# Kernel optimization log

Hardware: AMD Instinct MI355X
Metric: run time of the kernel (lower is better)

Reference implementation:

```python
import jax, jax.numpy as jnp
import numpy as np
import math

H, D, HID, L, OUT = 4, 64, 256, 2, 128
N = (2048, 4096, 3072)            # participant, gene, metabolite
IN_DIMS = (512, 768, 384)
# edge types: (src_type, dst_type, relation_index)
ETYPES = ((0, 1, 0), (1, 0, 1), (0, 2, 2), (2, 0, 3))
E_COUNTS = (250000, 250000, 200000, 200000)
SCALE = 1.0 / math.sqrt(D)


def _ln(x, g, b, eps=1e-5):
    m = x.mean(-1, keepdims=True)
    v = ((x - m) ** 2).mean(-1, keepdims=True)
    return (x - m) * jax.lax.rsqrt(v + eps) * g + b


def _cross_attn(qx, kvx, qw, qb, kw, kb, vw, vb, ow, ob):
    # qx: [Nq, HID] feature-node embeds (query); kvx: [Nk, HID] participant embeds
    Nq, Nk = qx.shape[0], kvx.shape[0]
    q = (qx @ qw + qb).reshape(Nq, H, D)
    k = (kvx @ kw + kb).reshape(Nk, H, D)
    v = (kvx @ vw + vb).reshape(Nk, H, D)
    att = jnp.einsum('qhd,khd->hqk', q, k) * SCALE
    p = jax.nn.softmax(att, axis=-1)
    o = jnp.einsum('hqk,khd->qhd', p, v).reshape(Nq, H * D)
    return o @ ow + ob


def _hgt_conv(hs, edges, kw, kb, qw, qb, vw, vb, aw, ab, skip, a_rel, m_rel, p_rel):
    # PyG-style HGTConv: per-type K/Q/V projections, per-relation a_rel/m_rel
    # transforms, segment softmax over all incoming edges per dst node.
    K = [(hs[t] @ kw[t] + kb[t]).reshape(N[t], H, D) for t in range(3)]
    Q = [(hs[t] @ qw[t] + qb[t]).reshape(N[t], H, D) for t in range(3)]
    V = [(hs[t] @ vw[t] + vb[t]).reshape(N[t], H, D) for t in range(3)]
    out = []
    for t in range(3):
        al, ms, ds = [], [], []
        for (s, d, r) in ETYPES:
            if d != t:
                continue
            src_idx, dst_idx = edges[r]
            k_e = jnp.einsum('ehd,hdf->ehf', K[s][src_idx], a_rel[r])  # [E,H,D]
            v_e = jnp.einsum('ehd,hdf->ehf', V[s][src_idx], m_rel[r])  # [E,H,D]
            a = (Q[t][dst_idx] * k_e).sum(-1) * (p_rel[r] * SCALE)     # [E,H]
            al.append(a); ms.append(v_e); ds.append(dst_idx)
        a = jnp.concatenate(al, 0)
        msg = jnp.concatenate(ms, 0)
        dst = jnp.concatenate(ds, 0)
        # numerically stable segment softmax grouped by destination node
        amax = jax.ops.segment_max(a, dst, num_segments=N[t])
        ex = jnp.exp(a - amax[dst])
        den = jax.ops.segment_sum(ex, dst, num_segments=N[t])
        w = ex / den[dst]                                             # [E,H]
        agg = jax.ops.segment_sum(w[..., None] * msg, dst,
                                  num_segments=N[t]).reshape(N[t], H * D)
        o = jax.nn.gelu(agg, approximate=False) @ aw[t] + ab[t]
        g = jax.nn.sigmoid(skip[t])
        out.append(g * o + (1.0 - g) * hs[t])
    return out


def _forward(x_p, x_g, x_m, edges, Win_p, bin_p, Win_g, bin_g, Win_m, bin_m,
             kw, kb, qw, qb, vw, vb, aw, ab, skip, a_rel, m_rel, p_rel,
             ca_qw, ca_qb, ca_kw, ca_kb, ca_vw, ca_vb, ca_ow, ca_ob,
             ln_g, ln_b, outw, outb):
    h = [x_p @ Win_p + bin_p, x_g @ Win_g + bin_g, x_m @ Win_m + bin_m]
    for l in range(L):
        hg = _hgt_conv(h, edges, kw[l], kb[l], qw[l], qb[l], vw[l], vb[l],
                       aw[l], ab[l], skip[l], a_rel[l], m_rel[l], p_rel[l])
        new = []
        for t in range(3):
            nh = hg[t]
            if t != 0:  # non-participant types cross-attend to participants
                c = t - 1
                nh = nh + _cross_attn(h[t], h[0], ca_qw[c], ca_qb[c],
                                      ca_kw[c], ca_kb[c], ca_vw[c], ca_vb[c],
                                      ca_ow[c], ca_ob[c])
            x = _ln(h[t] + nh, ln_g[t], ln_b[t])
            new.append(jax.nn.gelu(x, approximate=False))
        h = new
    return jnp.concatenate([h[t] @ outw[t] + outb[t] for t in range(3)], axis=0)


def setup_inputs() -> dict:
    key = jax.random.key(0)
    ks = iter(jax.random.split(key, 64))
    def nrm(shape, s=0.02):
        return jax.random.normal(next(ks), shape, dtype=jnp.float32) * s
    inp = {}
    inp['x_p'] = jax.random.normal(next(ks), (N[0], IN_DIMS[0]), dtype=jnp.float32)
    inp['x_g'] = jax.random.normal(next(ks), (N[1], IN_DIMS[1]), dtype=jnp.float32)
    inp['x_m'] = jax.random.normal(next(ks), (N[2], IN_DIMS[2]), dtype=jnp.float32)
    names = ('pg', 'gp', 'pm', 'mp')
    for (s, d, r), E in zip(ETYPES, E_COUNTS):
        inp['src_' + names[r]] = jax.random.randint(next(ks), (E,), 0, N[s], dtype=jnp.int32)
        inp['dst_' + names[r]] = jax.random.randint(next(ks), (E,), 0, N[d], dtype=jnp.int32)
    for nm, dim in (('p', 512), ('g', 768), ('m', 384)):
        inp['Win_' + nm] = nrm((dim, HID))
        inp['bin_' + nm] = jnp.zeros((HID,), jnp.float32)
    for nm in ('kw', 'qw', 'vw', 'aw'):
        inp[nm] = nrm((L, 3, HID, HID))
    for nm in ('kb', 'qb', 'vb', 'ab'):
        inp[nm] = jnp.zeros((L, 3, HID), jnp.float32)
    inp['skip'] = jnp.ones((L, 3), jnp.float32)
    inp['a_rel'] = nrm((L, 4, H, D, D), 0.1)
    inp['m_rel'] = nrm((L, 4, H, D, D), 0.1)
    inp['p_rel'] = jnp.ones((L, 4, H), jnp.float32)
    for nm in ('ca_qw', 'ca_kw', 'ca_vw', 'ca_ow'):
        inp[nm] = nrm((2, HID, HID))
    for nm in ('ca_qb', 'ca_kb', 'ca_vb', 'ca_ob'):
        inp[nm] = jnp.zeros((2, HID), jnp.float32)
    inp['ln_g'] = jnp.ones((3, HID), jnp.float32)
    inp['ln_b'] = jnp.zeros((3, HID), jnp.float32)
    inp['outw'] = nrm((3, HID, OUT))
    inp['outb'] = jnp.zeros((3, OUT), jnp.float32)
    return inp


def reference(x_p, x_g, x_m, src_pg, dst_pg, src_gp, dst_gp, src_pm, dst_pm,
              src_mp, dst_mp, Win_p, bin_p, Win_g, bin_g, Win_m, bin_m,
              kw, kb, qw, qb, vw, vb, aw, ab, skip, a_rel, m_rel, p_rel,
              ca_qw, ca_qb, ca_kw, ca_kb, ca_vw, ca_vb, ca_ow, ca_ob,
              ln_g, ln_b, outw, outb):
    edges = ((src_pg, dst_pg), (src_gp, dst_gp), (src_pm, dst_pm), (src_mp, dst_mp))
    return _forward(x_p, x_g, x_m, edges, Win_p, bin_p, Win_g, bin_g, Win_m, bin_m,
                    kw, kb, qw, qb, vw, vb, aw, ab, skip, a_rel, m_rel, p_rel,
                    ca_qw, ca_qb, ca_kw, ca_kb, ca_vw, ca_vb, ca_ow, ca_ob,
                    ln_g, ln_b, outw, outb)
```

## Files before the change

kernel.cpp:

```cpp
#include <hip/hip_runtime.h>
#include <math.h>
#include <stdint.h>
#include <stddef.h>

typedef unsigned short ushort_t;
typedef short  bf16x8 __attribute__((ext_vector_type(8)));
typedef float  f32x4  __attribute__((ext_vector_type(4)));
typedef unsigned short us4 __attribute__((ext_vector_type(4)));
typedef __bf16 bf16p2 __attribute__((ext_vector_type(2)));

static constexpr int NHEAD = 4;
static constexpr int HDIM  = 64;
static constexpr int HIDF  = 256;
static constexpr int OUTF  = 128;
static constexpr int N0 = 2048, N1 = 4096, N2 = 3072;
static constexpr int E_PG = 250000, E_GP = 250000, E_PM = 200000, E_MP = 200000;
static constexpr float ATT_SCALE = 0.125f;
static constexpr float LOG2E = 1.4426950408889634f;
static constexpr int EDGE_ITEMS = 2 * N0 + N1 + N2;
static constexpr int E_TOT = E_GP + E_MP + E_PG + E_PM;

enum { M_STORE = 0, M_ADD = 1, M_SKIP = 2, M_B16 = 3, M_GELU_B16 = 4,
       M_SPLITQ = 5, M_VT = 6, M_STOREBOTH = 7 };

__device__ __forceinline__ float gelu_exact(float x) {
    return 0.5f * x * (1.0f + erff(x * 0.7071067811865476f));
}
__device__ __forceinline__ ushort_t f2bf(float f) {
    unsigned x = __float_as_uint(f);
    return (ushort_t)((x + 0x7fffu + ((x >> 16) & 1u)) >> 16);
}
__device__ __forceinline__ float bflo(unsigned u) { return __uint_as_float(u << 16); }
__device__ __forceinline__ float bfhi(unsigned u) { return __uint_as_float(u & 0xffff0000u); }
__device__ __forceinline__ bf16p2 asbf2(unsigned u) { return __builtin_bit_cast(bf16p2, u); }

struct MGemmDesc { const ushort_t* A; const ushort_t* BT; void* C;
                   const float* bias; const float* skipv; void* H;
                   int M; int K; int mode; float scale; };
template <int NZ> struct MGemmDescArr { MGemmDesc d[NZ]; };

template <int NZ>
__global__ __launch_bounds__(256) void gemm_mfma(MGemmDescArr<NZ> P, int N)
{
    const MGemmDesc g = P.d[blockIdx.z];
    const int bm = blockIdx.y << 7;
    if (bm >= g.M) return;
    const int bn = blockIdx.x << 6;
    const int tid = threadIdx.x, wave = tid >> 6, lane = tid & 63;
    const int l15 = lane & 15, lg = lane >> 4;
    const int K = g.K;
    const ushort_t* arow = g.A + (size_t)(bm + (wave << 5) + l15) * K + (lg << 3);
    const ushort_t* brow = g.BT + (size_t)(bn + l15) * K + (lg << 3);

    f32x4 acc[2][4] = {};
    bf16x8 a0 = *(const bf16x8*)(arow);
    bf16x8 a1 = *(const bf16x8*)(arow + (size_t)16 * K);
    bf16x8 bv[4];
#pragma unroll
    for (int ct = 0; ct < 4; ct++)
        bv[ct] = *(const bf16x8*)(brow + (size_t)(ct << 4) * K);

    for (int k0 = 0; k0 < K; k0 += 32) {
        const bf16x8 ca0 = a0, ca1 = a1;
        bf16x8 cb[4];
#pragma unroll
        for (int ct = 0; ct < 4; ct++) cb[ct] = bv[ct];
        if (k0 + 32 < K) {
            a0 = *(const bf16x8*)(arow + k0 + 32);
            a1 = *(const bf16x8*)(arow + (size_t)16 * K + k0 + 32);
#pragma unroll
            for (int ct = 0; ct < 4; ct++)
                bv[ct] = *(const bf16x8*)(brow + (size_t)(ct << 4) * K + k0 + 32);
        }
#pragma unroll
        for (int ct = 0; ct < 4; ct++) {
            acc[0][ct] = __builtin_amdgcn_mfma_f32_16x16x32_bf16(ca0, cb[ct], acc[0][ct], 0, 0, 0);
            acc[1][ct] = __builtin_amdgcn_mfma_f32_16x16x32_bf16(ca1, cb[ct], acc[1][ct], 0, 0, 0);
        }
    }

    const int mode = g.mode;
    float gblend = 0.f, hblend = 0.f;
    if (mode == M_SKIP) {
        const float sv = g.skipv[0];
        gblend = 1.f / (1.f + expf(-sv));
        hblend = 1.f - gblend;
    }
#pragma unroll
    for (int g2 = 0; g2 < 2; g2++) {
        const int rbase = bm + (wave << 5) + (g2 << 4);
#pragma unroll
        for (int ct = 0; ct < 4; ct++) {
            const int col = bn + (ct << 4) + l15;
            const float bia = g.bias ? g.bias[col] : 0.f;
            if (mode == M_VT) {
                const int rowb = rbase + (lg << 2);
                us4 o;
#pragma unroll
                for (int r = 0; r < 4; r++) o[r] = f2bf(acc[g2][ct][r] + bia);
                *(us4*)((ushort_t*)g.C + (size_t)col * g.M + rowb) = o;
                continue;
            }
#pragma unroll
            for (int r = 0; r < 4; r++) {
                const int row = rbase + (lg << 2) + r;
                const float v = acc[g2][ct][r] + bia;
                if (mode == M_STORE) {
                    ((float*)g.C)[(size_t)row * N + col] = v;
                } else if (mode == M_ADD) {
                    ((float*)g.C)[(size_t)row * N + col] += v;
                } else if (mode == M_SKIP) {
                    ((float*)g.C)[(size_t)row * N + col] =
                        gblend * v + hblend * ((const float*)g.H)[(size_t)row * N + col];
                } else if (mode == M_B16) {
                    ((ushort_t*)g.C)[(size_t)row * N + col] = f2bf(v);
                } else if (mode == M_GELU_B16) {
                    ((ushort_t*)g.C)[(size_t)row * N + col] = f2bf(gelu_exact(v));
                } else if (mode == M_SPLITQ) {
                    ((ushort_t*)g.C)[((size_t)(col >> 6) * g.M + row) * 64 + (col & 63)]
                        = f2bf(v * g.scale);
                } else {
                    ((float*)g.C)[(size_t)row * N + col] = v;
                    ((ushort_t*)g.H)[(size_t)row * N + col] = f2bf(v);
                }
            }
        }
    }
}

struct TWDesc { const float* W; ushort_t* WT; int K; int N; };
template <int ND> struct TWDescArr { TWDesc d[ND]; };
struct QFDesc { const float* ar; const float* qwm; const float* qbv;
                ushort_t* wT; float* bT; };
template <int ND> struct QFDescArr { QFDesc d[ND]; };
struct MXDesc { const float* A; const float* B; ushort_t* out; int Kc; };
template <int ND> struct MXDescArr { MXDesc d[ND]; };

struct PreprocArgs {
    TWDescArr<32> T;
    QFDescArr<8> Q;
    MXDescArr<6> X;
    const float* xa; const float* xg; const float* xm; ushort_t* xb;
    int* cur_all;
};
static constexpr int PB_TW = 1536;
static constexpr int PB_QF = PB_TW + 32;
static constexpr int PB_MX = PB_QF + 3072;
static constexpr int PB_C3 = PB_MX + 5248;
static constexpr int PB_Z  = PB_C3 + 44;

__global__ __launch_bounds__(256) void preproc_kernel(PreprocArgs P)
{
    __shared__ __align__(16) char lsbuf[16640];
    const int b = blockIdx.x, tid = threadIdx.x;
    if (b < PB_TW) {
        const int z = b / 48, rem = b - z * 48;
        const int kx = rem % 12, ny = rem / 12;
        const TWDesc g = P.T.d[z];
        const int k0 = kx << 6, n0 = ny << 6;
        if (k0 >= g.K || n0 >= g.N) return;
        float (*Ls)[65] = (float (*)[65])lsbuf;
        const int c = tid & 63, rq = tid >> 6;
        for (int rr = rq; rr < 64; rr += 4)
            Ls[rr][c] = g.W[(size_t)(k0 + rr) * g.N + n0 + c];
        __syncthreads();
        for (int nn = rq; nn < 64; nn += 4)
            g.WT[(size_t)(n0 + nn) * g.K + k0 + c] = f2bf(Ls[c][nn]);
        return;
    }
    if (b < PB_QF) {
        const int idx = b - PB_TW;
        const int h = idx & 3, z = idx >> 2;
        const QFDesc g = P.Q.d[z];
        float (*arS)[64] = (float (*)[64])lsbuf;
        float* qbS = (float*)(lsbuf + 64 * 64 * 4);
        for (int i = tid; i < 4096; i += 256) arS[i >> 6][i & 63] = g.ar[(h << 12) + i];
        if (tid < 64) qbS[tid] = g.qbv[(h << 6) + tid];
        __syncthreads();
        float qv[64];
        const float* qrow = g.qwm + (size_t)tid * HIDF + (h << 6);
#pragma unroll
        for (int f = 0; f < 64; f++) qv[f] = qrow[f];
#pragma unroll 4
        for (int d = 0; d < 64; d++) {
            float a = 0.f;
#pragma unroll
            for (int f = 0; f < 64; f++) a = fmaf(arS[d][f], qv[f], a);
            g.wT[(size_t)((h << 6) + d) * HIDF + tid] = f2bf(a);
        }
        if (tid < 64) {
            float bb = 0.f;
#pragma unroll
            for (int f = 0; f < 64; f++) bb = fmaf(arS[tid][f], qbS[f], bb);
            g.bT[(h << 6) + tid] = bb;
        }
        return;
    }
    if (b < PB_MX) {
        const int idx0 = b - PB_QF;
        const int x = idx0 & 511, y = idx0 >> 9;
        const MXDesc g = P.X.d[y];
        const int idx = x * 256 + tid;
        if (idx >= 256 * g.Kc) return;
        const int col = idx / g.Kc, k = idx - col * g.Kc;
        const int h = col >> 6, f = col & 63;
        const float* M = g.A;
        int kd = k;
        if (k >= 256) { M = g.B; kd = k - 256; }
        const int hp = kd >> 6, d = kd & 63;
        const float v = (hp == h) ? M[(h << 12) + (d << 6) + f] : 0.f;
        g.out[idx] = f2bf(v);
        return;
    }
    if (b < PB_C3) {
        constexpr int n4a = N0 * 512 / 4, n4b = N1 * 768 / 4, n4c = N2 * 384 / 4;
        int i = (b - PB_MX) * 256 + tid;
        const float* src; int j;
        if (i < n4a) { src = P.xa; j = i; }
        else if (i < n4a + n4b) { src = P.xg; j = i - n4a; }
        else if (i < n4a + n4b + n4c) { src = P.xm; j = i - n4a - n4b; }
        else return;
        float4 v = ((const float4*)src)[j];
        us4 o;
        o[0] = f2bf(v.x); o[1] = f2bf(v.y); o[2] = f2bf(v.z); o[3] = f2bf(v.w);
        *(us4*)(P.xb + (size_t)i * 4) = o;
        return;
    }
    {
        int i = (b - PB_C3) * 256 + tid;
        if (i < 2 * N0 + N1 + N2) P.cur_all[i] = 0;
    }
}

__global__ void count4_kernel(const int* __restrict__ d0, const int* __restrict__ d1,
                              const int* __restrict__ d2, const int* __restrict__ d3,
                              int* __restrict__ c0, int* __restrict__ c1,
                              int* __restrict__ c2, int* __restrict__ c3)
{
    int i = blockIdx.x * 256 + threadIdx.x;
    if (i < E_GP) { atomicAdd(&c0[d0[i]], 1); return; }
    i -= E_GP;
    if (i < E_MP) { atomicAdd(&c1[d1[i]], 1); return; }
    i -= E_MP;
    if (i < E_PG) { atomicAdd(&c2[d2[i]], 1); return; }
    i -= E_PG;
    if (i < E_PM) atomicAdd(&c3[d3[i]], 1);
}

struct ScanDesc { int* cntcur; int N; int* off; };

__global__ __launch_bounds__(256) void scan4_kernel(ScanDesc s0, ScanDesc s1,
                                                    ScanDesc s2, ScanDesc s3)
{
    const ScanDesc g = (blockIdx.x == 0) ? s0 : (blockIdx.x == 1) ? s1
                     : (blockIdx.x == 2) ? s2 : s3;
    int* cntcur = g.cntcur; const int N = g.N; int* off = g.off;
    __shared__ int sums[256];
    const int tid = threadIdx.x;
    const int base = tid * 16;
    int vals[16];
    int s = 0;
#pragma unroll
    for (int j = 0; j < 16; j++) {
        int idx = base + j;
        int c = (idx < N) ? cntcur[idx] : 0;
        vals[j] = s; s += c;
    }
    sums[tid] = s;
    __syncthreads();
    for (int d = 1; d < 256; d <<= 1) {
        int v = (tid >= d) ? sums[tid - d] : 0;
        __syncthreads();
        sums[tid] += v;
        __syncthreads();
    }
    int prefix = (tid > 0) ? sums[tid - 1] : 0;
#pragma unroll
    for (int j = 0; j < 16; j++) {
        int idx = base + j;
        if (idx < N) { int v = prefix + vals[j]; off[idx] = v; cntcur[idx] = v; }
    }
    if (tid == 255) off[N] = sums[255];
}

__global__ void scatter4_kernel(
    const int* __restrict__ s0, const int* __restrict__ d0, int* __restrict__ u0, int* __restrict__ e0,
    const int* __restrict__ s1, const int* __restrict__ d1, int* __restrict__ u1, int* __restrict__ e1,
    const int* __restrict__ s2, const int* __restrict__ d2, int* __restrict__ u2, int* __restrict__ e2,
    const int* __restrict__ s3, const int* __restrict__ d3, int* __restrict__ u3, int* __restrict__ e3)
{
    int i = blockIdx.x * 256 + threadIdx.x;
    if (i < E_GP) { e0[atomicAdd(&u0[d0[i]], 1)] = s0[i]; return; }
    i -= E_GP;
    if (i < E_MP) { e1[atomicAdd(&u1[d1[i]], 1)] = s1[i]; return; }
    i -= E_MP;
    if (i < E_PG) { e2[atomicAdd(&u2[d2[i]], 1)] = s2[i]; return; }
    i -= E_PG;
    if (i < E_PM) e3[atomicAdd(&u3[d3[i]], 1)] = s3[i];
}

__device__ __forceinline__ void edge_seg_v9(
    const bf16p2* __restrict__ qd,
    float* __restrict__ sS,
    float2* __restrict__ wssh,
    const int* __restrict__ es, int i0, int i1,
    const ushort_t* __restrict__ Kt, const ushort_t* __restrict__ Vt,
    float pscale, int lane, int koff,
    float& m, float& plsum, float2& acc)
{
    if (i0 >= i1) return;
    const int seg = lane & 3, eidx = lane >> 2;
    const int epar = lane >> 5;
    const int dpair = (lane & 31) << 1;
    const int kbase_off = koff + (seg << 3);

    bool valid = (i0 + lane) < i1;
    int sidx = valid ? es[i0 + lane] : 0;
    uint4 kv[8];
#pragma unroll
    for (int p = 0; p < 4; p++) {
        const int sp = __shfl(sidx, (p << 4) + eidx);
        const ushort_t* kr = Kt + ((size_t)sp << 8) + kbase_off;
        kv[2 * p]     = *(const uint4*)(kr);
        kv[2 * p + 1] = *(const uint4*)(kr + 32);
    }

    for (int c = i0; c < i1; c += 64) {
        const int e2 = c + 64 + lane;
        const bool valid2 = e2 < i1;
        const int sidx2 = valid2 ? es[e2] : 0;

#pragma unroll
        for (int p = 0; p < 4; p++) {
            const uint4 k0 = kv[2 * p], k1 = kv[2 * p + 1];
            float dp = 0.f;
            dp = __builtin_amdgcn_fdot2_f32_bf16(asbf2(k0.x), qd[0], dp, false);
            dp = __builtin_amdgcn_fdot2_f32_bf16(asbf2(k0.y), qd[1], dp, false);
            dp = __builtin_amdgcn_fdot2_f32_bf16(asbf2(k0.z), qd[2], dp, false);
            dp = __builtin_amdgcn_fdot2_f32_bf16(asbf2(k0.w), qd[3], dp, false);
            dp = __builtin_amdgcn_fdot2_f32_bf16(asbf2(k1.x), qd[4], dp, false);
            dp = __builtin_amdgcn_fdot2_f32_bf16(asbf2(k1.y), qd[5], dp, false);
            dp = __builtin_amdgcn_fdot2_f32_bf16(asbf2(k1.z), qd[6], dp, false);
            dp = __builtin_amdgcn_fdot2_f32_bf16(asbf2(k1.w), qd[7], dp, false);
            dp += __shfl_xor(dp, 1);
            dp += __shfl_xor(dp, 2);
            if (seg == 0) sS[(p << 4) + eidx] = dp;
        }
#pragma unroll
        for (int p = 0; p < 4; p++) {
            const int sp = __shfl(sidx2, (p << 4) + eidx);
            const ushort_t* kr = Kt + ((size_t)sp << 8) + kbase_off;
            kv[2 * p]     = *(const uint4*)(kr);
            kv[2 * p + 1] = *(const uint4*)(kr + 32);
        }

        const float a = valid ? sS[lane] * pscale : -INFINITY;

        float cm = a;
#pragma unroll
        for (int o = 32; o; o >>= 1) cm = fmaxf(cm, __shfl_xor(cm, o));
        const float mn = fmaxf(m, cm);
        const float sc = (m == -INFINITY) ? 0.f : expf(m - mn);
        const float w = valid ? expf(a - mn) : 0.f;
        plsum = plsum * sc + w;
        m = mn;
        wssh[lane] = make_float2(w, __int_as_float(sidx));

        acc.x *= sc; acc.y *= sc;
        float2 aE = make_float2(0.f, 0.f), aO = make_float2(0.f, 0.f);
#pragma unroll
        for (int b = 0; b < 64; b += 16) {
            float2 we[8];
            unsigned vv[8];
#pragma unroll
            for (int j = 0; j < 8; j++) we[j] = wssh[b + (j << 1) + epar];
#pragma unroll
            for (int j = 0; j < 8; j++) {
                const int sj = __float_as_int(we[j].y);
                vv[j] = *(const unsigned*)(Vt + (((size_t)sj) << 8) + koff + dpair);
            }
#pragma unroll
            for (int j = 0; j < 8; j++) {
                const float wj = we[j].x;
                if (j & 1) { aO.x = fmaf(wj, bflo(vv[j]), aO.x);
                             aO.y = fmaf(wj, bfhi(vv[j]), aO.y); }
                else       { aE.x = fmaf(wj, bflo(vv[j]), aE.x);
                             aE.y = fmaf(wj, bfhi(vv[j]), aE.y); }
            }
        }
        acc.x += aE.x + aO.x;
        acc.y += aE.y + aO.y;

        valid = valid2; sidx = sidx2;
    }
}

__global__ __launch_bounds__(256) void edge_attn_v9(
    const float* __restrict__ QpDA, const float* __restrict__ QpDB,
    const float* __restrict__ QpS1, const float* __restrict__ QpS2,
    const int* __restrict__ offGP, const int* __restrict__ esGP,
    const int* __restrict__ offMP, const int* __restrict__ esMP,
    const int* __restrict__ offPG, const int* __restrict__ esPG,
    const int* __restrict__ offPM, const int* __restrict__ esPM,
    const ushort_t* __restrict__ K0t, const ushort_t* __restrict__ V0t,
    const ushort_t* __restrict__ K1t, const ushort_t* __restrict__ V1t,
    const ushort_t* __restrict__ K2t, const ushort_t* __restrict__ V2t,
    const float* __restrict__ prel,
    float* __restrict__ accD, float* __restrict__ mlD,
    ushort_t* __restrict__ out1, ushort_t* __restrict__ out2)
{
    __shared__ float sS[NHEAD][64];
    __shared__ float2 wssh[NHEAD][64];
    const int b = blockIdx.x, tid = threadIdx.x, lane = tid & 63, h = tid >> 6;
    const int koff = h << 6, seg = lane & 3;

    const float* Qp; const int* off; const int* es;
    const ushort_t* Kt; const ushort_t* Vt;
    int node, r, dual = -1;
    if (b < N0)            { node = b;            Qp = QpDA; off = offGP; es = esGP; Kt = K1t; Vt = V1t; r = 1; dual = 0; }
    else if (b < 2 * N0)   { node = b - N0;       Qp = QpDB; off = offMP; es = esMP; Kt = K2t; Vt = V2t; r = 3; dual = 1; }
    else if (b < 2 * N0 + N1) { node = b - 2 * N0;      Qp = QpS1; off = offPG; es = esPG; Kt = K0t; Vt = V0t; r = 0; }
    else                      { node = b - 2 * N0 - N1; Qp = QpS2; off = offPM; es = esPM; Kt = K0t; Vt = V0t; r = 2; }

    const float* qrow = Qp + (size_t)node * HIDF + koff;
    float4 qv[4];
    qv[0] = *(const float4*)(qrow + (seg << 3));
    qv[1] = *(const float4*)(qrow + (seg << 3) + 4);
    qv[2] = *(const float4*)(qrow + 32 + (seg << 3));
    qv[3] = *(const float4*)(qrow + 32 + (seg << 3) + 4);
    bf16p2 qd[8];
#pragma unroll
    for (int i = 0; i < 4; i++) {
        const unsigned p0 = (unsigned)f2bf(qv[i].x) | ((unsigned)f2bf(qv[i].y) << 16);
        const unsigned p1 = (unsigned)f2bf(qv[i].z) | ((unsigned)f2bf(qv[i].w) << 16);
        qd[2 * i]     = asbf2(p0);
        qd[2 * i + 1] = asbf2(p1);
    }
    const float ps = prel[(r << 2) + h] * ATT_SCALE;
    float m = -INFINITY, plsum = 0.f;
    float2 acc = make_float2(0.f, 0.f);
    edge_seg_v9(qd, sS[h], wssh[h], es, off[node], off[node + 1],
                Kt, Vt, ps, lane, koff, m, plsum, acc);
    acc.x += __shfl_xor(acc.x, 32);
    acc.y += __shfl_xor(acc.y, 32);
    float l = plsum;
#pragma unroll
    for (int o = 32; o; o >>= 1) l += __shfl_xor(l, o);

    if (dual >= 0) {
        if (lane < 32)
            *(float2*)(accD + ((size_t)(dual * N0 + node)) * HIDF + koff + ((lane & 31) << 1))
                = acc;
        if (lane == 0) {
            mlD[((size_t)(dual * N0 + node)) * 8 + h * 2 + 0] = m;
            mlD[((size_t)(dual * N0 + node)) * 8 + h * 2 + 1] = l;
        }
    } else {
        const float inv = (l > 0.f) ? 1.f / l : 0.f;
        ushort_t* out = (r == 0) ? out1 : out2;
        if (lane < 32) {
            const unsigned pk = (unsigned)f2bf(acc.x * inv) | ((unsigned)f2bf(acc.y * inv) << 16);
            *(unsigned*)(out + (size_t)node * HIDF + koff + ((lane & 31) << 1)) = pk;
        }
    }
}

__global__ __launch_bounds__(256) void combine0_kernel(
    const float* __restrict__ accD, const float* __restrict__ mlD,
    ushort_t* __restrict__ out0)
{
    const int node = blockIdx.x, col = threadIdx.x;
    const int h = col >> 6;
    const float m0 = mlD[((size_t)node) * 8 + h * 2 + 0];
    const float l0 = mlD[((size_t)node) * 8 + h * 2 + 1];
    const float m1 = mlD[((size_t)(N0 + node)) * 8 + h * 2 + 0];
    const float l1 = mlD[((size_t)(N0 + node)) * 8 + h * 2 + 1];
    const float M = fmaxf(m0, m1);
    const float s0 = (m0 == -INFINITY) ? 0.f : expf(m0 - M);
    const float s1 = (m1 == -INFINITY) ? 0.f : expf(m1 - M);
    const float L = l0 * s0 + l1 * s1;
    const float f0 = (L > 0.f) ? s0 / L : 0.f;
    const float f1 = (L > 0.f) ? s1 / L : 0.f;
    const float a0 = accD[((size_t)node) * HIDF + col];
    const float a1 = accD[((size_t)(N0 + node)) * HIDF + col];
    out0[(size_t)node * 512 + col]       = f2bf(a0 * f0);
    out0[(size_t)node * 512 + 256 + col] = f2bf(a1 * f1);
}

struct FlashDesc { const ushort_t* qh; const ushort_t* kh; const ushort_t* vT;
                   ushort_t* O; int Nq; };
template <int NF> struct FlashDescArr { FlashDesc d[NF]; };

template <int NF>
__global__ __launch_bounds__(256) void flash_ca(FlashDescArr<NF> P, int Nk)
{
    const FlashDesc g = P.d[blockIdx.z];
    const int q0 = blockIdx.x << 5;
    if (q0 >= g.Nq) return;
    __shared__ float mS[4][32], lS[4][32];
    __shared__ __align__(16) char uS[18432];
    ushort_t (*Pl)[32][72] = (ushort_t (*)[32][72])uS;
    float    (*oS)[16][64] = (float (*)[16][64])uS;
    const int head = blockIdx.y;
    const int tid = threadIdx.x, wave = tid >> 6, lane = tid & 63;
    const int l15 = lane & 15, lg = lane >> 4;
    const int Nq = g.Nq;

    bf16x8 qa[2][2];
    {
        const ushort_t* qb0 = g.qh + ((size_t)head * Nq + q0 + l15) * 64 + (lg << 3);
        qa[0][0] = *(const bf16x8*)qb0;
        qa[0][1] = *(const bf16x8*)(qb0 + 32);
        qa[1][0] = *(const bf16x8*)(qb0 + 16 * 64);
        qa[1][1] = *(const bf16x8*)(qb0 + 16 * 64 + 32);
    }
    const ushort_t* kbase = g.kh + (size_t)head * Nk * 64;
    const ushort_t* vbase = g.vT + (size_t)head * 64 * Nk;
    const int kchunk = Nk >> 2;
    const int kbeg = wave * kchunk, kend = kbeg + kchunk;

    f32x4 o[2][4] = {};
    float m[2][4]     = {{-INFINITY,-INFINITY,-INFINITY,-INFINITY},
                         {-INFINITY,-INFINITY,-INFINITY,-INFINITY}};
    float plsum[2][4] = {};

    bf16x8 ka[8];
    {
        const ushort_t* krow = kbase + ((size_t)(kbeg + l15)) * 64 + (lg << 3);
#pragma unroll
        for (int ct = 0; ct < 4; ct++) {
            ka[ct]     = *(const bf16x8*)(krow + (ct << 10));
            ka[4 + ct] = *(const bf16x8*)(krow + (ct << 10) + 32);
        }
    }

    for (int k0 = kbeg; k0 < kend; k0 += 64) {
        bf16x8 vv[8];
        const ushort_t* vrow = vbase + (size_t)l15 * Nk + k0 + (lg << 3);
#pragma unroll
        for (int vt = 0; vt < 4; vt++) {
            vv[vt]     = *(const bf16x8*)(vrow + (size_t)(vt << 4) * Nk);
            vv[4 + vt] = *(const bf16x8*)(vrow + (size_t)(vt << 4) * Nk + 32);
        }
        f32x4 s[2][4] = {};
#pragma unroll
        for (int g2 = 0; g2 < 2; g2++)
#pragma unroll
            for (int ct = 0; ct < 4; ct++)
                s[g2][ct] = __builtin_amdgcn_mfma_f32_16x16x32_bf16(qa[g2][0], ka[ct], s[g2][ct], 0, 0, 0);
#pragma unroll
        for (int g2 = 0; g2 < 2; g2++)
#pragma unroll
            for (int ct = 0; ct < 4; ct++)
                s[g2][ct] = __builtin_amdgcn_mfma_f32_16x16x32_bf16(qa[g2][1], ka[4 + ct], s[g2][ct], 0, 0, 0);
        if (k0 + 64 < kend) {
            const ushort_t* krow2 = kbase + ((size_t)(k0 + 64 + l15)) * 64 + (lg << 3);
#pragma unroll
            for (int ct = 0; ct < 4; ct++) {
                ka[ct]     = *(const bf16x8*)(krow2 + (ct << 10));
                ka[4 + ct] = *(const bf16x8*)(krow2 + (ct << 10) + 32);
            }
        }
        float tm[2][4];
        bool need = false;
#pragma unroll
        for (int g2 = 0; g2 < 2; g2++)
#pragma unroll
            for (int r = 0; r < 4; r++) {
                tm[g2][r] = fmaxf(fmaxf(s[g2][0][r], s[g2][1][r]),
                                  fmaxf(s[g2][2][r], s[g2][3][r]));
                need = need || (tm[g2][r] > m[g2][r] + 11.54f);
            }
        if (__any(need)) {
#pragma unroll
            for (int off = 1; off <= 8; off <<= 1)
#pragma unroll
                for (int g2 = 0; g2 < 2; g2++)
#pragma unroll
                    for (int r = 0; r < 4; r++)
                        tm[g2][r] = fmaxf(tm[g2][r], __shfl_xor(tm[g2][r], off));
#pragma unroll
            for (int g2 = 0; g2 < 2; g2++)
#pragma unroll
                for (int r = 0; r < 4; r++) {
                    const float mn = fmaxf(m[g2][r], tm[g2][r]);
                    const float sc = exp2f(m[g2][r] - mn);
                    m[g2][r] = mn;
                    plsum[g2][r] *= sc;
#pragma unroll
                    for (int vt = 0; vt < 4; vt++) o[g2][vt][r] *= sc;
                }
        }
#pragma unroll
        for (int g2 = 0; g2 < 2; g2++)
#pragma unroll
            for (int ct = 0; ct < 4; ct++)
#pragma unroll
                for (int r = 0; r < 4; r++) {
                    const float p = exp2f(s[g2][ct][r] - m[g2][r]);
                    plsum[g2][r] += p;
                    Pl[wave][(g2 << 4) + (lg << 2) + r][(ct << 4) + l15] = f2bf(p);
                }
        const bf16x8 pa00 = *(const bf16x8*)&Pl[wave][l15][lg << 3];
        const bf16x8 pa01 = *(const bf16x8*)&Pl[wave][l15][32 + (lg << 3)];
        const bf16x8 pa10 = *(const bf16x8*)&Pl[wave][16 + l15][lg << 3];
        const bf16x8 pa11 = *(const bf16x8*)&Pl[wave][16 + l15][32 + (lg << 3)];
#pragma unroll
        for (int vt = 0; vt < 4; vt++) {
            o[0][vt] = __builtin_amdgcn_mfma_f32_16x16x32_bf16(pa00, vv[vt], o[0][vt], 0, 0, 0);
            o[1][vt] = __builtin_amdgcn_mfma_f32_16x16x32_bf16(pa10, vv[vt], o[1][vt], 0, 0, 0);
        }
#pragma unroll
        for (int vt = 0; vt < 4; vt++) {
            o[0][vt] = __builtin_amdgcn_mfma_f32_16x16x32_bf16(pa01, vv[4 + vt], o[0][vt], 0, 0, 0);
            o[1][vt] = __builtin_amdgcn_mfma_f32_16x16x32_bf16(pa11, vv[4 + vt], o[1][vt], 0, 0, 0);
        }
    }
#pragma unroll
    for (int off = 1; off <= 8; off <<= 1)
#pragma unroll
        for (int g2 = 0; g2 < 2; g2++)
#pragma unroll
            for (int r = 0; r < 4; r++)
                plsum[g2][r] += __shfl_xor(plsum[g2][r], off);
    if (l15 == 0) {
#pragma unroll
        for (int g2 = 0; g2 < 2; g2++)
#pragma unroll
            for (int r = 0; r < 4; r++) {
                mS[wave][(g2 << 4) + (lg << 2) + r] = m[g2][r];
                lS[wave][(g2 << 4) + (lg << 2) + r] = plsum[g2][r];
            }
    }
    __syncthreads();
#pragma unroll
    for (int g2 = 0; g2 < 2; g2++) {
        float fac[4];
#pragma unroll
        for (int r = 0; r < 4; r++) {
            const int grow = (g2 << 4) + (lg << 2) + r;
            const float ms = fmaxf(fmaxf(mS[0][grow], mS[1][grow]),
                                   fmaxf(mS[2][grow], mS[3][grow]));
            fac[r] = exp2f(m[g2][r] - ms);
        }
        __syncthreads();
#pragma unroll
        for (int vt = 0; vt < 4; vt++)
#pragma unroll
            for (int r = 0; r < 4; r++)
                oS[wave][(lg << 2) + r][(vt << 4) + l15] = o[g2][vt][r] * fac[r];
        __syncthreads();
        for (int i = tid; i < 1024; i += 256) {
            const int row = i >> 6, d = i & 63;
            const int grow = (g2 << 4) + row;
            const float m0 = mS[0][grow], m1 = mS[1][grow], m2 = mS[2][grow], m3 = mS[3][grow];
            const float ms = fmaxf(fmaxf(m0, m1), fmaxf(m2, m3));
            const float L = lS[0][grow] * exp2f(m0 - ms) + lS[1][grow] * exp2f(m1 - ms)
                          + lS[2][grow] * exp2f(m2 - ms) + lS[3][grow] * exp2f(m3 - ms);
            const float val = oS[0][row][d] + oS[1][row][d] + oS[2][row][d] + oS[3][row][d];
            g.O[(size_t)(q0 + grow) * HIDF + (head << 6) + d] = f2bf(val / L);
        }
    }
}

__global__ __launch_bounds__(256) void ln_gelu_all(
    float* __restrict__ h, ushort_t* __restrict__ hb16, const float* __restrict__ hg,
    const float* __restrict__ lng, const float* __restrict__ lnb)
{
    __shared__ float t4[4];
    const int row = blockIdx.x, tid = threadIdx.x, lane = tid & 63, w = tid >> 6;
    const int t = (row >= N0) + (row >= N0 + N1);
    const size_t idx = (size_t)row * HIDF + tid;
    const float x = h[idx] + hg[idx];
    float v = x;
#pragma unroll
    for (int o = 32; o; o >>= 1) v += __shfl_xor(v, o);
    if (lane == 0) t4[w] = v;
    __syncthreads();
    const float mean = (t4[0] + t4[1] + t4[2] + t4[3]) * (1.f / 256.f);
    __syncthreads();
    const float d = x - mean;
    v = d * d;
#pragma unroll
    for (int o = 32; o; o >>= 1) v += __shfl_xor(v, o);
    if (lane == 0) t4[w] = v;
    __syncthreads();
    const float var = (t4[0] + t4[1] + t4[2] + t4[3]) * (1.f / 256.f);
    const float y = gelu_exact(d * rsqrtf(var + 1e-5f) * lng[t * HIDF + tid] + lnb[t * HIDF + tid]);
    h[idx] = y;
    hb16[idx] = f2bf(y);
}

extern "C" void kernel_launch(void* const* d_in, const int* in_sizes, int n_in,
                              void* d_out, int out_size, void* d_ws, size_t ws_size,
                              hipStream_t stream)
{
    (void)in_sizes; (void)n_in; (void)out_size; (void)ws_size;
    const float* x_p   = (const float*)d_in[0];
    const float* x_g   = (const float*)d_in[1];
    const float* x_m   = (const float*)d_in[2];
    const int*  src_pg = (const int*)d_in[3];
    const int*  dst_pg = (const int*)d_in[4];
    const int*  src_gp = (const int*)d_in[5];
    const int*  dst_gp = (const int*)d_in[6];
    const int*  src_pm = (const int*)d_in[7];
    const int*  dst_pm = (const int*)d_in[8];
    const int*  src_mp = (const int*)d_in[9];
    const int*  dst_mp = (const int*)d_in[10];
    const float* Win_p = (const float*)d_in[11];
    const float* bin_p = (const float*)d_in[12];
    const float* Win_g = (const float*)d_in[13];
    const float* bin_g = (const float*)d_in[14];
    const float* Win_m = (const float*)d_in[15];
    const float* bin_m = (const float*)d_in[16];
    const float* kw    = (const float*)d_in[17];
    const float* qw    = (const float*)d_in[18];
    const float* vw    = (const float*)d_in[19];
    const float* aw    = (const float*)d_in[20];
    const float* kb    = (const float*)d_in[21];
    const float* qb    = (const float*)d_in[22];
    const float* vb    = (const float*)d_in[23];
    const float* ab    = (const float*)d_in[24];
    const float* skip  = (const float*)d_in[25];
    const float* a_rel = (const float*)d_in[26];
    const float* m_rel = (const float*)d_in[27];
    const float* p_rel = (const float*)d_in[28];
    const float* ca_qw = (const float*)d_in[29];
    const float* ca_kw = (const float*)d_in[30];
    const float* ca_vw = (const float*)d_in[31];
    const float* ca_ow = (const float*)d_in[32];
    const float* ca_qb = (const float*)d_in[33];
    const float* ca_kb = (const float*)d_in[34];
    const float* ca_vb = (const float*)d_in[35];
    const float* ca_ob = (const float*)d_in[36];
    const float* ln_g  = (const float*)d_in[37];
    const float* ln_b  = (const float*)d_in[38];
    const float* outw  = (const float*)d_in[39];
    const float* outb  = (const float*)d_in[40];
    float* dout = (float*)d_out;

    float* Wp = (float*)d_ws;
    size_t cursz = 0;
    auto alloc = [&](size_t n) -> float* {
        float* p = Wp + cursz; cursz += (n + 63) & ~(size_t)63; return p;
    };
    const size_t NT = N0 + N1 + N2;
    float* h0  = alloc((size_t)N0 * HIDF);
    float* h1  = alloc((size_t)N1 * HIDF);
    float* h2  = alloc((size_t)N2 * HIDF);
    float* hg0 = alloc((size_t)N0 * HIDF);
    float* hg1 = alloc((size_t)N1 * HIDF);
    float* hg2 = alloc((size_t)N2 * HIDF);
    ushort_t* hb  = (ushort_t*)alloc(NT * HIDF / 2);
    ushort_t* K16 = (ushort_t*)alloc(NT * HIDF / 2);
    ushort_t* V16 = (ushort_t*)alloc(NT * HIDF / 2);
    ushort_t* K16_0 = K16, *K16_1 = K16 + (size_t)N0 * HIDF, *K16_2 = K16 + (size_t)(N0 + N1) * HIDF;
    ushort_t* V16_0 = V16, *V16_1 = V16 + (size_t)N0 * HIDF, *V16_2 = V16 + (size_t)(N0 + N1) * HIDF;
    float* QpPool  = alloc((size_t)(N1 + N0 + N2 + N0) * HIDF);
    float* Qp0 = QpPool;
    float* Qp1 = Qp0 + (size_t)N1 * HIDF;
    float* Qp2 = Qp1 + (size_t)N0 * HIDF;
    float* Qp3 = Qp2 + (size_t)N2 * HIDF;
    float* accD = alloc((size_t)2 * N0 * HIDF);
    float* mlD  = alloc((size_t)2 * N0 * 8);
    ushort_t* part0b = (ushort_t*)alloc((size_t)N0 * 512 / 2);
    ushort_t* part1b = (ushort_t*)alloc((size_t)N1 * HIDF / 2);
    ushort_t* part2b = (ushort_t*)alloc((size_t)N2 * HIDF / 2);
    ushort_t* aggb16 = (ushort_t*)alloc(NT * HIDF / 2);
    ushort_t* qhA   = (ushort_t*)alloc((size_t)N1 * HIDF / 2);
    ushort_t* qhB   = (ushort_t*)alloc((size_t)N2 * HIDF / 2);
    ushort_t* khA   = (ushort_t*)alloc((size_t)N0 * HIDF / 2);
    ushort_t* khB   = (ushort_t*)alloc((size_t)N0 * HIDF / 2);
    ushort_t* vTA   = (ushort_t*)alloc((size_t)N0 * HIDF / 2);
    ushort_t* vTB   = (ushort_t*)alloc((size_t)N0 * HIDF / 2);
    ushort_t* caobA = (ushort_t*)alloc((size_t)N1 * HIDF / 2);
    ushort_t* caobB = (ushort_t*)alloc((size_t)N2 * HIDF / 2);
    ushort_t* WT16 = (ushort_t*)alloc(2621440 / 2);
    ushort_t* WqpT = (ushort_t*)alloc((size_t)8 * 65536 / 2);
    float*    bqp  = alloc(8 * 256);
    ushort_t* WmT  = (ushort_t*)alloc((size_t)2 * 262144 / 2);
    ushort_t* xb = (ushort_t*)QpPool;
    int* es_gp = (int*)alloc(E_GP);
    int* es_mp = (int*)alloc(E_MP);
    int* es_pg = (int*)alloc(E_PG);
    int* es_pm = (int*)alloc(E_PM);
    int* off_gp = (int*)alloc(N0 + 1);
    int* off_mp = (int*)alloc(N0 + 1);
    int* off_pg = (int*)alloc(N1 + 1);
    int* off_pm = (int*)alloc(N2 + 1);
    int* cur_all = (int*)alloc(2 * N0 + N1 + N2);
    int* cur_gp = cur_all;
    int* cur_mp = cur_all + N0;
    int* cur_pg = cur_all + 2 * N0;
    int* cur_pm = cur_all + 2 * N0 + N1;

    ushort_t* kwT    = WT16;
    ushort_t* vwT    = WT16 + 6 * 65536;
    ushort_t* awT    = WT16 + 12 * 65536;
    ushort_t* ca_qwT = WT16 + 18 * 65536;
    ushort_t* ca_kwT = WT16 + 20 * 65536;
    ushort_t* ca_vwT = WT16 + 22 * 65536;
    ushort_t* ca_owT = WT16 + 24 * 65536;
    ushort_t* outwT  = WT16 + 26 * 65536;
    ushort_t* WinTp  = outwT + 3 * 32768;
    ushort_t* WinTg  = WinTp + 256 * 512;
    ushort_t* WinTm  = WinTg + 256 * 768;

    ushort_t* WmT_l[2][3];
    {
        PreprocArgs P;
        for (int i = 0; i < 6; i++) {
            P.T.d[i]      = { kw + (size_t)i * 65536, kwT + (size_t)i * 65536, 256, 256 };
            P.T.d[6 + i]  = { vw + (size_t)i * 65536, vwT + (size_t)i * 65536, 256, 256 };
            P.T.d[12 + i] = { aw + (size_t)i * 65536, awT + (size_t)i * 65536, 256, 256 };
        }
        for (int c = 0; c < 2; c++) {
            P.T.d[18 + c] = { ca_qw + (size_t)c * 65536, ca_qwT + (size_t)c * 65536, 256, 256 };
            P.T.d[20 + c] = { ca_kw + (size_t)c * 65536, ca_kwT + (size_t)c * 65536, 256, 256 };
            P.T.d[22 + c] = { ca_vw + (size_t)c * 65536, ca_vwT + (size_t)c * 65536, 256, 256 };
            P.T.d[24 + c] = { ca_ow + (size_t)c * 65536, ca_owT + (size_t)c * 65536, 256, 256 };
        }
        for (int t = 0; t < 3; t++)
            P.T.d[26 + t] = { outw + (size_t)t * 32768, outwT + (size_t)t * 32768, 256, 128 };
        P.T.d[29] = { Win_p, WinTp, 512, 256 };
        P.T.d[30] = { Win_g, WinTg, 768, 256 };
        P.T.d[31] = { Win_m, WinTm, 384, 256 };

        const int dstt[4] = { 1, 0, 2, 0 };
        for (int l = 0; l < 2; l++)
            for (int r = 0; r < 4; r++) {
                const int z = l * 4 + r, dt = dstt[r];
                P.Q.d[z] = { a_rel + (size_t)z * 16384,
                             qw + (size_t)(l * 3 + dt) * 65536,
                             qb + (size_t)(l * 3 + dt) * 256,
                             WqpT + (size_t)z * 65536, bqp + (size_t)z * 256 };
            }

        for (int l = 0; l < 2; l++) {
            ushort_t* base = WmT + (size_t)l * 262144;
            WmT_l[l][0] = base;
            WmT_l[l][1] = base + 131072;
            WmT_l[l][2] = base + 196608;
            const float* mr = m_rel + (size_t)l * 4 * 16384;
            P.X.d[l * 3 + 0] = { mr + 1 * 16384, mr + 3 * 16384, WmT_l[l][0], 512 };
            P.X.d[l * 3 + 1] = { mr + 0 * 16384, nullptr,        WmT_l[l][1], 256 };
            P.X.d[l * 3 + 2] = { mr + 2 * 16384, nullptr,        WmT_l[l][2], 256 };
        }
        P.xa = x_p; P.xg = x_g; P.xm = x_m; P.xb = xb;
        P.cur_all = cur_all;
        preproc_kernel<<<PB_Z, 256, 0, stream>>>(P);
    }

    count4_kernel<<<(E_TOT + 255) / 256, 256, 0, stream>>>(
        dst_gp, dst_mp, dst_pg, dst_pm, cur_gp, cur_mp, cur_pg, cur_pm);
    {
        ScanDesc s0 = { cur_gp, N0, off_gp };
        ScanDesc s1 = { cur_mp, N0, off_mp };
        ScanDesc s2 = { cur_pg, N1, off_pg };
        ScanDesc s3 = { cur_pm, N2, off_pm };
        scan4_kernel<<<4, 256, 0, stream>>>(s0, s1, s2, s3);
    }
    scatter4_kernel<<<(E_TOT + 255) / 256, 256, 0, stream>>>(
        src_gp, dst_gp, cur_gp, es_gp,
        src_mp, dst_mp, cur_mp, es_mp,
        src_pg, dst_pg, cur_pg, es_pg,
        src_pm, dst_pm, cur_pm, es_pm);

    float* hgptr[3] = { hg0, hg1, hg2 };
    float* hptr[3]  = { h0, h1, h2 };
    const int Ns[3] = { N0, N1, N2 };
    const size_t hoff[3] = { 0, (size_t)N0 * HIDF, (size_t)(N0 + N1) * HIDF };

    const size_t xoff1 = (size_t)N0 * 512, xoff2 = xoff1 + (size_t)N1 * 768;
    {
        MGemmDescArr<3> D;
        D.d[0] = { xb,         WinTp, h0, bin_p, nullptr, hb + hoff[0], N0, 512, M_STOREBOTH, 0.f };
        D.d[1] = { xb + xoff1, WinTg, h1, bin_g, nullptr, hb + hoff[1], N1, 768, M_STOREBOTH, 0.f };
        D.d[2] = { xb + xoff2, WinTm, h2, bin_m, nullptr, hb + hoff[2], N2, 384, M_STOREBOTH, 0.f };
        gemm_mfma<3><<<dim3(4, 32, 3), 256, 0, stream>>>(D, HIDF);
    }

    for (int l = 0; l < 2; l++) {
        {
            ushort_t* Kp[3] = { K16_0, K16_1, K16_2 };
            ushort_t* Vp[3] = { V16_0, V16_1, V16_2 };
            const size_t zb = (size_t)l * 4;
            MGemmDescArr<10> D;
            D.d[0] = { hb + hoff[1], WqpT + (zb + 0) * 65536, Qp0, bqp + (zb + 0) * 256, nullptr, nullptr, N1, HIDF, M_STORE, 0.f };
            D.d[1] = { hb + hoff[0], WqpT + (zb + 1) * 65536, Qp1, bqp + (zb + 1) * 256, nullptr, nullptr, N0, HIDF, M_STORE, 0.f };
            D.d[2] = { hb + hoff[2], WqpT + (zb + 2) * 65536, Qp2, bqp + (zb + 2) * 256, nullptr, nullptr, N2, HIDF, M_STORE, 0.f };
            D.d[3] = { hb + hoff[0], WqpT + (zb + 3) * 65536, Qp3, bqp + (zb + 3) * 256, nullptr, nullptr, N0, HIDF, M_STORE, 0.f };
            for (int t = 0; t < 3; t++) {
                D.d[4 + t] = { hb + hoff[t], kwT + (size_t)(l * 3 + t) * 65536, Kp[t],
                               kb + (size_t)(l * 3 + t) * HIDF, nullptr, nullptr, Ns[t], HIDF, M_B16, 0.f };
                D.d[7 + t] = { hb + hoff[t], vwT + (size_t)(l * 3 + t) * 65536, Vp[t],
                               vb + (size_t)(l * 3 + t) * HIDF, nullptr, nullptr, Ns[t], HIDF, M_B16, 0.f };
            }
            gemm_mfma<10><<<dim3(4, 32, 10), 256, 0, stream>>>(D, HIDF);
        }
        const float* prl = p_rel + (size_t)l * 16;
        edge_attn_v9<<<EDGE_ITEMS, 256, 0, stream>>>(
            Qp1, Qp3, Qp0, Qp2,
            off_gp, es_gp, off_mp, es_mp, off_pg, es_pg, off_pm, es_pm,
            K16_0, V16_0, K16_1, V16_1, K16_2, V16_2,
            prl, accD, mlD, part1b, part2b);
        combine0_kernel<<<N0, 256, 0, stream>>>(accD, mlD, part0b);
        {
            MGemmDescArr<3> D;
            D.d[0] = { part0b, WmT_l[l][0], aggb16 + hoff[0], nullptr, nullptr, nullptr, N0, 512, M_GELU_B16, 0.f };
            D.d[1] = { part1b, WmT_l[l][1], aggb16 + hoff[1], nullptr, nullptr, nullptr, N1, 256, M_GELU_B16, 0.f };
            D.d[2] = { part2b, WmT_l[l][2], aggb16 + hoff[2], nullptr, nullptr, nullptr, N2, 256, M_GELU_B16, 0.f };
            gemm_mfma<3><<<dim3(4, 32, 3), 256, 0, stream>>>(D, HIDF);
        }
        {
            MGemmDescArr<9> D;
            for (int t = 0; t < 3; t++)
                D.d[t] = { aggb16 + hoff[t], awT + (size_t)(l * 3 + t) * 65536, hgptr[t],
                           ab + (size_t)(l * 3 + t) * HIDF, skip + l * 3 + t, hptr[t], Ns[t], HIDF, M_SKIP, 0.f };
            D.d[3] = { hb + hoff[1], ca_qwT + 0 * 65536, qhA, ca_qb + 0 * HIDF, nullptr, nullptr, N1, HIDF, M_SPLITQ, ATT_SCALE * LOG2E };
            D.d[4] = { hb + hoff[0], ca_kwT + 0 * 65536, khA, ca_kb + 0 * HIDF, nullptr, nullptr, N0, HIDF, M_SPLITQ, 1.0f };
            D.d[5] = { hb + hoff[0], ca_vwT + 0 * 65536, vTA, ca_vb + 0 * HIDF, nullptr, nullptr, N0, HIDF, M_VT, 0.f };
            D.d[6] = { hb + hoff[2], ca_qwT + 1 * 65536, qhB, ca_qb + 1 * HIDF, nullptr, nullptr, N2, HIDF, M_SPLITQ, ATT_SCALE * LOG2E };
            D.d[7] = { hb + hoff[0], ca_kwT + 1 * 65536, khB, ca_kb + 1 * HIDF, nullptr, nullptr, N0, HIDF, M_SPLITQ, 1.0f };
            D.d[8] = { hb + hoff[0], ca_vwT + 1 * 65536, vTB, ca_vb + 1 * HIDF, nullptr, nullptr, N0, HIDF, M_VT, 0.f };
            gemm_mfma<9><<<dim3(4, 32, 9), 256, 0, stream>>>(D, HIDF);
        }
        {
            FlashDescArr<2> F;
            F.d[0] = { qhA, khA, vTA, caobA, N1 };
            F.d[1] = { qhB, khB, vTB, caobB, N2 };
            flash_ca<2><<<dim3(N1 / 32, NHEAD, 2), 256, 0, stream>>>(F, N0);
        }
        {
            MGemmDescArr<2> D;
            D.d[0] = { caobA, ca_owT + 0 * 65536, hg1, ca_ob + 0 * HIDF, nullptr, nullptr, N1, HIDF, M_ADD, 0.f };
            D.d[1] = { caobB, ca_owT + 1 * 65536, hg2, ca_ob + 1 * HIDF, nullptr, nullptr, N2, HIDF, M_ADD, 0.f };
            gemm_mfma<2><<<dim3(4, 32, 2), 256, 0, stream>>>(D, HIDF);
        }

        ln_gelu_all<<<(int)NT, 256, 0, stream>>>(h0, hb, hg0, ln_g, ln_b);
    }

    {
        MGemmDescArr<3> D;
        D.d[0] = { hb + hoff[0], outwT + 0,     dout,                            outb,       nullptr, nullptr, N0, HIDF, M_STORE, 0.f };
        D.d[1] = { hb + hoff[1], outwT + 32768, dout + (size_t)N0 * OUTF,        outb + 128, nullptr, nullptr, N1, HIDF, M_STORE, 0.f };
        D.d[2] = { hb + hoff[2], outwT + 65536, dout + (size_t)(N0 + N1) * OUTF, outb + 256, nullptr, nullptr, N2, HIDF, M_STORE, 0.f };
        gemm_mfma<3><<<dim3(2, 32, 3), 256, 0, stream>>>(D, OUTF);
    }
}
```

Measured before the change: 799.9 us.

## Enlarge GEMM wave tile to 64x64 with double-buffered K-step of 64

Each wave now computes a 64x64 output tile (4x4 MFMA accumulators) instead of 32x64, and the block covers 256 rows. The K loop processes two 32-wide slices per iteration with register double buffering. All grid y-dimensions are halved to match. The goal is better operand reuse per global load; the cost is more registers and fewer blocks, which may reduce occupancy and CU coverage for these small GEMMs.

```diff
diff --git a/kernel.cpp b/kernel.cpp
--- a/kernel.cpp
+++ b/kernel.cpp
@@ -43,40 +43,46 @@
 __global__ __launch_bounds__(256) void gemm_mfma(MGemmDescArr<NZ> P, int N)
 {
     const MGemmDesc g = P.d[blockIdx.z];
-    const int bm = blockIdx.y << 7;
+    const int bm = blockIdx.y << 8;
     if (bm >= g.M) return;
     const int bn = blockIdx.x << 6;
     const int tid = threadIdx.x, wave = tid >> 6, lane = tid & 63;
     const int l15 = lane & 15, lg = lane >> 4;
     const int K = g.K;
-    const ushort_t* arow = g.A + (size_t)(bm + (wave << 5) + l15) * K + (lg << 3);
+    const ushort_t* arow = g.A + (size_t)(bm + (wave << 6) + l15) * K + (lg << 3);
     const ushort_t* brow = g.BT + (size_t)(bn + l15) * K + (lg << 3);
 
-    f32x4 acc[2][4] = {};
-    bf16x8 a0 = *(const bf16x8*)(arow);
-    bf16x8 a1 = *(const bf16x8*)(arow + (size_t)16 * K);
-    bf16x8 bv[4];
-#pragma unroll
-    for (int ct = 0; ct < 4; ct++)
-        bv[ct] = *(const bf16x8*)(brow + (size_t)(ct << 4) * K);
-
-    for (int k0 = 0; k0 < K; k0 += 32) {
-        const bf16x8 ca0 = a0, ca1 = a1;
-        bf16x8 cb[4];
-#pragma unroll
-        for (int ct = 0; ct < 4; ct++) cb[ct] = bv[ct];
-        if (k0 + 32 < K) {
-            a0 = *(const bf16x8*)(arow + k0 + 32);
-            a1 = *(const bf16x8*)(arow + (size_t)16 * K + k0 + 32);
-#pragma unroll
-            for (int ct = 0; ct < 4; ct++)
-                bv[ct] = *(const bf16x8*)(brow + (size_t)(ct << 4) * K + k0 + 32);
-        }
-#pragma unroll
-        for (int ct = 0; ct < 4; ct++) {
-            acc[0][ct] = __builtin_amdgcn_mfma_f32_16x16x32_bf16(ca0, cb[ct], acc[0][ct], 0, 0, 0);
-            acc[1][ct] = __builtin_amdgcn_mfma_f32_16x16x32_bf16(ca1, cb[ct], acc[1][ct], 0, 0, 0);
-        }
+    f32x4 acc[4][4] = {};
+    bf16x8 a0[4], b0[4], a1[4], b1[4];
+#pragma unroll
+    for (int i = 0; i < 4; i++) {
+        a0[i] = *(const bf16x8*)(arow + (size_t)(i << 4) * K);
+        b0[i] = *(const bf16x8*)(brow + (size_t)(i << 4) * K);
+    }
+
+    for (int k0 = 0; k0 < K; k0 += 64) {
+#pragma unroll
+        for (int i = 0; i < 4; i++) {
+            a1[i] = *(const bf16x8*)(arow + (size_t)(i << 4) * K + k0 + 32);
+            b1[i] = *(const bf16x8*)(brow + (size_t)(i << 4) * K + k0 + 32);
+        }
+#pragma unroll
+        for (int ct = 0; ct < 4; ct++)
+#pragma unroll
+            for (int ar = 0; ar < 4; ar++)
+                acc[ar][ct] = __builtin_amdgcn_mfma_f32_16x16x32_bf16(a0[ar], b0[ct], acc[ar][ct], 0, 0, 0);
+        if (k0 + 64 < K) {
+#pragma unroll
+            for (int i = 0; i < 4; i++) {
+                a0[i] = *(const bf16x8*)(arow + (size_t)(i << 4) * K + k0 + 64);
+                b0[i] = *(const bf16x8*)(brow + (size_t)(i << 4) * K + k0 + 64);
+            }
+        }
+#pragma unroll
+        for (int ct = 0; ct < 4; ct++)
+#pragma unroll
+            for (int ar = 0; ar < 4; ar++)
+                acc[ar][ct] = __builtin_amdgcn_mfma_f32_16x16x32_bf16(a1[ar], b1[ct], acc[ar][ct], 0, 0, 0);
     }
 
     const int mode = g.mode;
@@ -87,8 +93,8 @@
         hblend = 1.f - gblend;
     }
 #pragma unroll
-    for (int g2 = 0; g2 < 2; g2++) {
-        const int rbase = bm + (wave << 5) + (g2 << 4);
+    for (int g2 = 0; g2 < 4; g2++) {
+        const int rbase = bm + (wave << 6) + (g2 << 4);
 #pragma unroll
         for (int ct = 0; ct < 4; ct++) {
             const int col = bn + (ct << 4) + l15;
@@ -877,7 +883,7 @@
         D.d[0] = { xb,         WinTp, h0, bin_p, nullptr, hb + hoff[0], N0, 512, M_STOREBOTH, 0.f };
         D.d[1] = { xb + xoff1, WinTg, h1, bin_g, nullptr, hb + hoff[1], N1, 768, M_STOREBOTH, 0.f };
         D.d[2] = { xb + xoff2, WinTm, h2, bin_m, nullptr, hb + hoff[2], N2, 384, M_STOREBOTH, 0.f };
-        gemm_mfma<3><<<dim3(4, 32, 3), 256, 0, stream>>>(D, HIDF);
+        gemm_mfma<3><<<dim3(4, 16, 3), 256, 0, stream>>>(D, HIDF);
     }
 
     for (int l = 0; l < 2; l++) {
@@ -896,7 +902,7 @@
                 D.d[7 + t] = { hb + hoff[t], vwT + (size_t)(l * 3 + t) * 65536, Vp[t],
                                vb + (size_t)(l * 3 + t) * HIDF, nullptr, nullptr, Ns[t], HIDF, M_B16, 0.f };
             }
-            gemm_mfma<10><<<dim3(4, 32, 10), 256, 0, stream>>>(D, HIDF);
+            gemm_mfma<10><<<dim3(4, 16, 10), 256, 0, stream>>>(D, HIDF);
         }
         const float* prl = p_rel + (size_t)l * 16;
         edge_attn_v9<<<EDGE_ITEMS, 256, 0, stream>>>(
@@ -910,7 +916,7 @@
             D.d[0] = { part0b, WmT_l[l][0], aggb16 + hoff[0], nullptr, nullptr, nullptr, N0, 512, M_GELU_B16, 0.f };
             D.d[1] = { part1b, WmT_l[l][1], aggb16 + hoff[1], nullptr, nullptr, nullptr, N1, 256, M_GELU_B16, 0.f };
             D.d[2] = { part2b, WmT_l[l][2], aggb16 + hoff[2], nullptr, nullptr, nullptr, N2, 256, M_GELU_B16, 0.f };
-            gemm_mfma<3><<<dim3(4, 32, 3), 256, 0, stream>>>(D, HIDF);
+            gemm_mfma<3><<<dim3(4, 16, 3), 256, 0, stream>>>(D, HIDF);
         }
         {
             MGemmDescArr<9> D;
@@ -923,7 +929,7 @@
             D.d[6] = { hb + hoff[2], ca_qwT + 1 * 65536, qhB, ca_qb + 1 * HIDF, nullptr, nullptr, N2, HIDF, M_SPLITQ, ATT_SCALE * LOG2E };
             D.d[7] = { hb + hoff[0], ca_kwT + 1 * 65536, khB, ca_kb + 1 * HIDF, nullptr, nullptr, N0, HIDF, M_SPLITQ, 1.0f };
             D.d[8] = { hb + hoff[0], ca_vwT + 1 * 65536, vTB, ca_vb + 1 * HIDF, nullptr, nullptr, N0, HIDF, M_VT, 0.f };
-            gemm_mfma<9><<<dim3(4, 32, 9), 256, 0, stream>>>(D, HIDF);
+            gemm_mfma<9><<<dim3(4, 16, 9), 256, 0, stream>>>(D, HIDF);
         }
         {
             FlashDescArr<2> F;
@@ -935,7 +941,7 @@
             MGemmDescArr<2> D;
             D.d[0] = { caobA, ca_owT + 0 * 65536, hg1, ca_ob + 0 * HIDF, nullptr, nullptr, N1, HIDF, M_ADD, 0.f };
             D.d[1] = { caobB, ca_owT + 1 * 65536, hg2, ca_ob + 1 * HIDF, nullptr, nullptr, N2, HIDF, M_ADD, 0.f };
-            gemm_mfma<2><<<dim3(4, 32, 2), 256, 0, stream>>>(D, HIDF);
+            gemm_mfma<2><<<dim3(4, 16, 2), 256, 0, stream>>>(D, HIDF);
         }
 
         ln_gelu_all<<<(int)NT, 256, 0, stream>>>(h0, hb, hg0, ln_g, ln_b);
@@ -946,6 +952,6 @@
         D.d[0] = { hb + hoff[0], outwT + 0,     dout,                            outb,       nullptr, nullptr, N0, HIDF, M_STORE, 0.f };
         D.d[1] = { hb + hoff[1], outwT + 32768, dout + (size_t)N0 * OUTF,        outb + 128, nullptr, nullptr, N1, HIDF, M_STORE, 0.f };
         D.d[2] = { hb + hoff[2], outwT + 65536, dout + (size_t)(N0 + N1) * OUTF, outb + 256, nullptr, nullptr, N2, HIDF, M_STORE, 0.f };
-        gemm_mfma<3><<<dim3(2, 32, 3), 256, 0, stream>>>(D, OUTF);
-    }
-}
+        gemm_mfma<3><<<dim3(2, 16, 3), 256, 0, stream>>>(D, OUTF);
+    }
+}
```

Result: slower. 866.0 us (+8.3%).
